# Performance work log

Hardware: AMD Instinct MI355X
Metric: run time of the kernel (lower is better)

The kernel has to match this reference:

```python
import jax, jax.numpy as jnp
import numpy as np

EPS = 1e-5  # BatchNorm eps


def _unfold3x3(x):
    """torch.nn.Unfold(kernel=3, pad=1, stride=1) -> [B, H*W, 9, C] layout.

    Kernel positions are row-major (kh, kw); index 4 is the center, matching
    x_pn[:, :, 4:5, :] in the torch module.
    """
    B, C, H, W = x.shape
    xp = jnp.pad(x, ((0, 0), (0, 0), (1, 1), (1, 1)))
    patches = jnp.stack([xp[:, :, i:i + H, j:j + W]
                         for i in range(3) for j in range(3)], axis=1)  # [B,9,C,H,W]
    return patches.transpose(0, 3, 4, 1, 2).reshape(B, H * W, 9, C)


def setup_inputs() -> dict:
    key = jax.random.key(0)
    ks = jax.random.split(key, 10)
    B, Cin, Cout, H, W = 2, 64, 64, 64, 2048
    Ctot = 4 + Cin  # 4 meta channels + feature channels
    return {
        "x": jax.random.normal(ks[0], (B, Ctot, H, W), jnp.float32),
        "mask": jax.random.randint(ks[1], (B, 1, H, W), 0, 2, jnp.int32),
        # weight_mlp1: Linear(4 -> Cin, bias=False), torch layout [out, in]
        "W1": jax.random.normal(ks[2], (Cin, 4), jnp.float32) * 0.3,
        "bn1_g": jnp.ones((Cin,), jnp.float32),
        "bn1_b": jnp.zeros((Cin,), jnp.float32),
        "bn1_m": jax.random.normal(ks[3], (Cin,), jnp.float32) * 0.1,
        "bn1_v": jax.random.uniform(ks[4], (Cin,), jnp.float32, 0.5, 1.5),
        # weight_mlp2: Linear(Cin -> 1) (attention head)
        "W2": jax.random.normal(ks[5], (1, Cin), jnp.float32) * 0.1,
        "b2": jnp.zeros((1,), jnp.float32),
        # aggregation_mlp: Linear(9*Cin -> Cout, bias=False)
        "Wagg": jax.random.normal(ks[6], (Cout, 9 * Cin), jnp.float32) * 0.04,
        "bn2_g": jnp.ones((Cout,), jnp.float32),
        "bn2_b": jnp.zeros((Cout,), jnp.float32),
        "bn2_m": jax.random.normal(ks[7], (Cout,), jnp.float32) * 0.1,
        "bn2_v": jax.random.uniform(ks[8], (Cout,), jnp.float32, 0.5, 1.5),
    }


def reference(x, mask, W1, bn1_g, bn1_b, bn1_m, bn1_v, W2, b2,
              Wagg, bn2_g, bn2_b, bn2_m, bn2_v):
    B, Ctot, H, W_ = x.shape
    Cin = W1.shape[0]

    xu = _unfold3x3(x)                       # [B, HW, 9, Ctot]
    feats = xu[..., 4:]                      # [B, HW, 9, Cin]
    pn = xu[..., :4]                         # meta coords of 9 neighbors
    d = pn - pn[:, :, 4:5, :]                # relative to center pixel

    # per-neighbor weight MLP (Linear -> BN(eval) -> ReLU -> Linear)
    w = jnp.einsum('bnkm,cm->bnkc', d, W1)   # [B, HW, 9, Cin]
    w = (w - bn1_m) * (bn1_g * jax.lax.rsqrt(bn1_v + EPS)) + bn1_b
    w = jax.nn.relu(w)
    w = jnp.einsum('bnkc,oc->bnko', w, W2) + b2  # [B, HW, 9, 1]

    mu = _unfold3x3(mask.astype(jnp.float32))    # [B, HW, 9, 1]
    w = w * mu                                   # masked logits
    w = jax.nn.softmax(w[..., 0], axis=-1)[..., None]  # attention over 9 neighbors

    out = (w * feats).reshape(B, H * W_, 9 * Cin)
    y = jnp.einsum('bnf,of->bno', out, Wagg)     # [B, HW, Cout]
    y = (y - bn2_m) * (bn2_g * jax.lax.rsqrt(bn2_v + EPS)) + bn2_b
    y = jax.nn.relu(y)
    # Fold(kernel=1) == reshape back to the feature map
    return y.transpose(0, 2, 1).reshape(B, -1, H, W_)
```

## Files before the change

### kernel.cpp

```cpp
#include <hip/hip_runtime.h>

#define H_ 64
#define W_ 2048
#define HWsz (H_*W_)
#define CIN 64
#define CTOT 68
#define COUT 64

typedef float  f32x4  __attribute__((ext_vector_type(4)));
typedef float  f32x16 __attribute__((ext_vector_type(16)));
typedef short  s16x8  __attribute__((ext_vector_type(8)));

__device__ __forceinline__ unsigned short f2bf(float f) {
    unsigned u = __builtin_bit_cast(unsigned, f);
    unsigned r = u + 0x7fffu + ((u >> 16) & 1u);
    return (unsigned short)(r >> 16);
}

__global__ __launch_bounds__(256) void prep_bw(
    const float* __restrict__ Wagg, unsigned short* __restrict__ BwS)
{
    int idx = blockIdx.x * 256 + threadIdx.x;
    if (idx >= 4608) return;
    int lane = idx & 63;
    int rest = idx >> 6;
    int nt = rest & 1;
    int ks = (rest >> 1) & 3;
    int k9 = rest >> 3;
    int o  = nt*32 + (lane & 31);
    int ch = ks*16 + (lane >> 5)*8;
    const float* src = Wagg + (size_t)o*(9*CIN) + k9*64 + ch;
    s16x8 v8;
#pragma unroll
    for (int j = 0; j < 8; ++j) v8[j] = (short)f2bf(src[j]);
    *(s16x8*)(BwS + (size_t)idx*8) = v8;
}

__global__ __launch_bounds__(256, 4) void wsoft_k(
    const float* __restrict__ x, const int* __restrict__ mask,
    const float* __restrict__ W1, const float* __restrict__ g1,
    const float* __restrict__ b1, const float* __restrict__ m1,
    const float* __restrict__ v1, const float* __restrict__ W2,
    const float* __restrict__ b2p, float* __restrict__ wbuf)
{
    __shared__ float pos[3][4][260];
    __shared__ float musk[3][260];
    __shared__ float Wc[64][8];

    int tid = threadIdx.x;
    int bx = blockIdx.x, by = blockIdx.y;
    int b = by >> 6, h = by & 63;
    int w0 = bx << 8;
    const float* xb = x + (size_t)b * CTOT * HWsz;

#pragma unroll
    for (int it = 0; it < 3; ++it) {
        int i = it*256 + tid;
        int grp = i & 63;
        int rc = i >> 6;
        int ch = rc & 3, r = rc >> 2;
        int gr = h - 1 + r;
        float4 v = {0.f, 0.f, 0.f, 0.f};
        if ((unsigned)gr < (unsigned)H_)
            v = *(const float4*)(xb + (size_t)ch*HWsz + (size_t)gr*W_ + w0 + grp*4);
        float* dst = &pos[r][ch][1 + grp*4];
        dst[0] = v.x; dst[1] = v.y; dst[2] = v.z; dst[3] = v.w;
    }
    if (tid < 192) {
        int grp = tid & 63, r = tid >> 6;
        int gr = h - 1 + r;
        float4 mv = {0.f, 0.f, 0.f, 0.f};
        if ((unsigned)gr < (unsigned)H_) {
            const int* mp = mask + ((size_t)b*H_ + gr)*W_ + w0 + grp*4;
            mv.x = (float)mp[0]; mv.y = (float)mp[1]; mv.z = (float)mp[2]; mv.w = (float)mp[3];
        }
        float* dst = &musk[r][1 + grp*4];
        dst[0] = mv.x; dst[1] = mv.y; dst[2] = mv.z; dst[3] = mv.w;
    }
    if (tid < 24) {
        int c2 = tid & 1;
        int rc = tid >> 1; int ch = rc & 3, r = rc >> 2;
        int gr = h - 1 + r, gc = w0 - 1 + c2*257;
        float v = 0.f;
        if (((unsigned)gr < (unsigned)H_) && ((unsigned)gc < (unsigned)W_))
            v = xb[(size_t)ch*HWsz + (size_t)gr*W_ + gc];
        pos[r][ch][c2*257] = v;
    }
    if (tid >= 32 && tid < 38) {
        int t = tid - 32;
        int c2 = t & 1, r = t >> 1;
        int gr = h - 1 + r, gc = w0 - 1 + c2*257;
        float v = 0.f;
        if (((unsigned)gr < (unsigned)H_) && ((unsigned)gc < (unsigned)W_))
            v = (float)mask[((size_t)b*H_ + gr)*W_ + gc];
        musk[r][c2*257] = v;
    }
    if (tid >= 64 && tid < 128) {
        int c = tid - 64;
        float s1 = g1[c] * rsqrtf(v1[c] + 1e-5f);
#pragma unroll
        for (int m = 0; m < 4; ++m) Wc[c][m] = W1[c*4 + m] * s1;
        Wc[c][4] = b1[c] - m1[c]*s1;
        Wc[c][5] = W2[c];
    }
    __syncthreads();

    int px = tid;
    float pc[4];
#pragma unroll
    for (int m = 0; m < 4; ++m) pc[m] = pos[1][m][1 + px];
    float d[9][4], mu[9];
#pragma unroll
    for (int k = 0; k < 9; ++k) {
        int r = k/3, dw = k%3 - 1;
#pragma unroll
        for (int m = 0; m < 4; ++m) d[k][m] = pos[r][m][1 + px + dw] - pc[m];
        mu[k] = musk[r][1 + px + dw];
    }

    float lg[9];
#pragma unroll
    for (int k = 0; k < 9; ++k) lg[k] = 0.f;

#pragma unroll 4
    for (int c = 0; c < CIN; ++c) {
        f32x4 wv = *(const f32x4*)&Wc[c][0];
        float t1c = Wc[c][4], w2c = Wc[c][5];
#pragma unroll
        for (int k = 0; k < 9; ++k) {
            float v = fmaf(d[k][0], wv[0], fmaf(d[k][1], wv[1],
                      fmaf(d[k][2], wv[2], fmaf(d[k][3], wv[3], t1c))));
            lg[k] += fmaxf(v, 0.f) * w2c;
        }
    }

    float b2v = b2p[0];
    float mx = -1e30f;
#pragma unroll
    for (int k = 0; k < 9; ++k) { lg[k] = (lg[k] + b2v) * mu[k]; mx = fmaxf(mx, lg[k]); }
    float s = 0.f, e[9];
#pragma unroll
    for (int k = 0; k < 9; ++k) { e[k] = __expf(lg[k] - mx); s += e[k]; }
    float inv = 1.f / s;
#pragma unroll
    for (int k = 0; k < 9; ++k)
        wbuf[((size_t)by*9 + k)*W_ + w0 + px] = e[k] * inv;
}

__global__ __launch_bounds__(256, 4) void agg_k(
    const float* __restrict__ x,
    const unsigned short* __restrict__ BwS,
    const float* __restrict__ wbuf,
    const float* __restrict__ g2, const float* __restrict__ bb2,
    const float* __restrict__ m2, const float* __restrict__ v2,
    float* __restrict__ out)
{
    __shared__ __align__(16) unsigned short fe[3][8][66][8];

    int tid = threadIdx.x;
    int bx = blockIdx.x, by = blockIdx.y;
    int b = by >> 6, h = by & 63;
    int w0 = bx << 6;
    const float* xf = x + ((size_t)b*CTOT + 4) * HWsz;

#pragma unroll
    for (int it = 0; it < 6; ++it) {
        int i = it*256 + tid;
        int col = i & 63;
        int rg = i >> 6;
        int g = rg & 7, r = rg >> 3;
        int gr = h - 1 + r;
        s16x8 v8 = {0,0,0,0,0,0,0,0};
        if ((unsigned)gr < (unsigned)H_) {
            const float* src = xf + (size_t)(g*8)*HWsz + (size_t)gr*W_ + w0 + col;
#pragma unroll
            for (int j = 0; j < 8; ++j) v8[j] = (short)f2bf(src[(size_t)j*HWsz]);
        }
        *(s16x8*)&fe[r][g][1 + col][0] = v8;
    }
    if (tid < 48) {
        int c2 = tid & 1;
        int rg = tid >> 1;
        int g = rg & 7, r = rg >> 3;
        int gr = h - 1 + r;
        int gc = w0 - 1 + c2*65;
        s16x8 v8 = {0,0,0,0,0,0,0,0};
        if (((unsigned)gr < (unsigned)H_) && ((unsigned)gc < (unsigned)W_)) {
            const float* src = xf + (size_t)(g*8)*HWsz + (size_t)gr*W_ + gc;
#pragma unroll
            for (int j = 0; j < 8; ++j) v8[j] = (short)f2bf(src[(size_t)j*HWsz]);
        }
        *(s16x8*)&fe[r][g][c2*65][0] = v8;
    }
    __syncthreads();

    int lane = tid & 63, wv = tid >> 6;
    int nt = wv & 1, mq = wv >> 1;
    int l31 = lane & 31, l5 = lane >> 5;

    f32x16 fin = {0.f,0.f,0.f,0.f,0.f,0.f,0.f,0.f,0.f,0.f,0.f,0.f,0.f,0.f,0.f,0.f};
    const float* wrow = wbuf + (size_t)by*9*W_ + w0 + mq*32 + 4*l5;

#pragma unroll
    for (int k9 = 0; k9 < 9; ++k9) {
        const int r = k9/3, dw = k9%3 - 1;
        int col = 1 + mq*32 + l31 + dw;

        s16x8 bf[4], af[4];
#pragma unroll
        for (int ks = 0; ks < 4; ++ks)
            bf[ks] = *(const s16x8*)(BwS + (size_t)((((k9<<2) + ks)*2 + nt) << 9) + lane*8);
#pragma unroll
        for (int ks = 0; ks < 4; ++ks)
            af[ks] = *(const s16x8*)&fe[r][ks*2 + l5][col][0];

        f32x16 tmp = {0.f,0.f,0.f,0.f,0.f,0.f,0.f,0.f,0.f,0.f,0.f,0.f,0.f,0.f,0.f,0.f};
#pragma unroll
        for (int ks = 0; ks < 4; ++ks)
            tmp = __builtin_amdgcn_mfma_f32_32x32x16_bf16(af[ks], bf[ks], tmp, 0, 0, 0);

        const float* wk = wrow + (size_t)k9*W_;
        f32x4 a0 = *(const f32x4*)(wk);
        f32x4 a1 = *(const f32x4*)(wk + 8);
        f32x4 a2 = *(const f32x4*)(wk + 16);
        f32x4 a3 = *(const f32x4*)(wk + 24);
#pragma unroll
        for (int c = 0; c < 4; ++c) {
            fin[c]      += a0[c] * tmp[c];
            fin[4 + c]  += a1[c] * tmp[4 + c];
            fin[8 + c]  += a2[c] * tmp[8 + c];
            fin[12 + c] += a3[c] * tmp[12 + c];
        }
    }

    int o = nt*32 + l31;
    float sc = g2[o] * rsqrtf(v2[o] + 1e-5f);
    float tc = bb2[o] - m2[o]*sc;
    float* orow = out + (((size_t)b*COUT + o)*H_ + h)*W_ + w0 + mq*32 + 4*l5;
#pragma unroll
    for (int v = 0; v < 4; ++v) {
        f32x4 q;
#pragma unroll
        for (int c = 0; c < 4; ++c) q[c] = fmaxf(fmaf(fin[4*v + c], sc, tc), 0.f);
        *(f32x4*)(orow + 8*v) = q;
    }
}

extern "C" void kernel_launch(void* const* d_in, const int* in_sizes, int n_in,
                              void* d_out, int out_size, void* d_ws, size_t ws_size,
                              hipStream_t stream)
{
    const float* x    = (const float*)d_in[0];
    const int*   mask = (const int*)d_in[1];
    const float* W1   = (const float*)d_in[2];
    const float* g1   = (const float*)d_in[3];
    const float* b1   = (const float*)d_in[4];
    const float* m1   = (const float*)d_in[5];
    const float* v1   = (const float*)d_in[6];
    const float* W2   = (const float*)d_in[7];
    const float* b2   = (const float*)d_in[8];
    const float* Wagg = (const float*)d_in[9];
    const float* g2   = (const float*)d_in[10];
    const float* bb2  = (const float*)d_in[11];
    const float* m2   = (const float*)d_in[12];
    const float* v2   = (const float*)d_in[13];
    float* outp = (float*)d_out;

    char* ws = (char*)d_ws;
    unsigned short* BwS = (unsigned short*)(ws + 0);
    float* wbuf = (float*)(ws + 131072);

    hipLaunchKernelGGL(prep_bw, dim3(18), dim3(256), 0, stream, Wagg, BwS);
    hipLaunchKernelGGL(wsoft_k, dim3(W_/256, 128), dim3(256), 0, stream,
                       x, mask, W1, g1, b1, m1, v1, W2, b2, wbuf);
    hipLaunchKernelGGL(agg_k, dim3(W_/64, 128), dim3(256), 0, stream,
                       x, BwS, wbuf, g2, bb2, m2, v2, outp);
}
```

Before: 228.8 us.

## Pre-pack features into padded bf16 channel-grouped layout and widen aggregation tiles

Adds a prep kernel that converts the feature channels into a zero-padded bf16 layout grouped by 8 channels. A new aggregation kernel then loads these tiles straight into LDS with global_load_lds, with no per-element conversion or bounds checks, and covers 128 columns per block. It also skips the center-neighbor MLP in wsoft_k, because d=0 there gives a constant logit that is precomputed per channel. The cost is an extra full pass over x (read fp32, write bf16) plus a roughly 35MB workspace, and the old path is kept as a fallback when the workspace is too small.

```diff
diff --git a/kernel.cpp b/kernel.cpp
--- a/kernel.cpp
+++ b/kernel.cpp
@@ -6,6 +6,9 @@
 #define CIN 64
 #define CTOT 68
 #define COUT 64
+
+#define XH 66
+#define XW 2050
 
 typedef float  f32x4  __attribute__((ext_vector_type(4)));
 typedef float  f32x16 __attribute__((ext_vector_type(16)));
@@ -36,6 +39,28 @@
     *(s16x8*)(BwS + (size_t)idx*8) = v8;
 }
 
+__global__ __launch_bounds__(256) void prep_x(
+    const float* __restrict__ x, unsigned short* __restrict__ xpad)
+{
+    int wc = blockIdx.x * 256 + threadIdx.x;
+    if (wc >= XW) return;
+    int hr = blockIdx.y;
+    int b  = blockIdx.z;
+    bool interior = (hr >= 1) && (hr <= H_) && (wc >= 1) && (wc <= W_);
+    const float* src0 = x + ((size_t)b*CTOT + 4)*HWsz + (size_t)(hr-1)*W_ + (wc-1);
+    unsigned short* dst0 = xpad + ((((size_t)b*XH + hr)*8)*XW + wc)*8;
+#pragma unroll
+    for (int g = 0; g < 8; ++g) {
+        s16x8 v8 = {0,0,0,0,0,0,0,0};
+        if (interior) {
+            const float* s = src0 + (size_t)(g*8)*HWsz;
+#pragma unroll
+            for (int j = 0; j < 8; ++j) v8[j] = (short)f2bf(s[(size_t)j*HWsz]);
+        }
+        *(s16x8*)(dst0 + (size_t)g*XW*8) = v8;
+    }
+}
+
 __global__ __launch_bounds__(256, 4) void wsoft_k(
     const float* __restrict__ x, const int* __restrict__ mask,
     const float* __restrict__ W1, const float* __restrict__ g1,
@@ -100,8 +125,12 @@
         float s1 = g1[c] * rsqrtf(v1[c] + 1e-5f);
 #pragma unroll
         for (int m = 0; m < 4; ++m) Wc[c][m] = W1[c*4 + m] * s1;
-        Wc[c][4] = b1[c] - m1[c]*s1;
-        Wc[c][5] = W2[c];
+        float t1c = b1[c] - m1[c]*s1;
+        float w2c = W2[c];
+        Wc[c][4] = t1c;
+        Wc[c][5] = w2c;
+        Wc[c][6] = fmaxf(t1c, 0.f) * w2c;
+        Wc[c][7] = 0.f;
     }
     __syncthreads();
 
@@ -121,18 +150,22 @@
     float lg[9];
 #pragma unroll
     for (int k = 0; k < 9; ++k) lg[k] = 0.f;
+    float lg4 = 0.f;
 
 #pragma unroll 4
     for (int c = 0; c < CIN; ++c) {
         f32x4 wv = *(const f32x4*)&Wc[c][0];
-        float t1c = Wc[c][4], w2c = Wc[c][5];
-#pragma unroll
-        for (int k = 0; k < 9; ++k) {
+        f32x4 w2 = *(const f32x4*)&Wc[c][4];
+        lg4 += w2[2];
+#pragma unroll
+        for (int kk = 0; kk < 8; ++kk) {
+            const int k = kk + (kk >= 4);
             float v = fmaf(d[k][0], wv[0], fmaf(d[k][1], wv[1],
-                      fmaf(d[k][2], wv[2], fmaf(d[k][3], wv[3], t1c))));
-            lg[k] += fmaxf(v, 0.f) * w2c;
-        }
-    }
+                      fmaf(d[k][2], wv[2], fmaf(d[k][3], wv[3], w2[0]))));
+            lg[k] += fmaxf(v, 0.f) * w2[1];
+        }
+    }
+    lg[4] = lg4;
 
     float b2v = b2p[0];
     float mx = -1e30f;
@@ -145,6 +178,99 @@
 #pragma unroll
     for (int k = 0; k < 9; ++k)
         wbuf[((size_t)by*9 + k)*W_ + w0 + px] = e[k] * inv;
+}
+
+__global__ __launch_bounds__(256, 3) void agg_k2(
+    const unsigned short* __restrict__ xpad,
+    const unsigned short* __restrict__ BwS,
+    const float* __restrict__ wbuf,
+    const float* __restrict__ g2, const float* __restrict__ bb2,
+    const float* __restrict__ m2, const float* __restrict__ v2,
+    float* __restrict__ out)
+{
+    __shared__ __align__(16) unsigned short fe[3][8][130][8];
+
+    int tid = threadIdx.x;
+    int bx = blockIdx.x, by = blockIdx.y;
+    int b = by >> 6, h = by & 63;
+    int w0 = bx << 7;
+    int lane = tid & 63, wv = tid >> 6;
+
+    const unsigned short* xb = xpad + (size_t)b*XH*8*XW*8;
+
+#pragma unroll
+    for (int it = 0; it < 12; ++it) {
+        int u = it*4 + wv;
+        int chunk = u & 1, g = (u >> 1) & 7, r = u >> 4;
+        const unsigned short* gsrc =
+            xb + ((((size_t)(h + r)*8 + g)*XW) + w0 + 1 + chunk*64 + lane)*8;
+        unsigned short* ldst = &fe[r][g][1 + chunk*64][0];
+        __builtin_amdgcn_global_load_lds(
+            (const __attribute__((address_space(1))) unsigned int*)gsrc,
+            (__attribute__((address_space(3))) unsigned int*)ldst, 16, 0, 0);
+    }
+    if (tid < 48) {
+        int c2 = tid & 1, g = (tid >> 1) & 7, r = tid >> 4;
+        int wc = w0 + c2*129;
+        s16x8 v8 = *(const s16x8*)(xb + ((((size_t)(h + r)*8 + g)*XW) + wc)*8);
+        *(s16x8*)&fe[r][g][c2*129][0] = v8;
+    }
+    __syncthreads();
+
+    int nt = wv & 1, mh = wv >> 1;
+    int l31 = lane & 31, l5 = lane >> 5;
+
+    const f32x16 fz16 = {0.f,0.f,0.f,0.f,0.f,0.f,0.f,0.f,0.f,0.f,0.f,0.f,0.f,0.f,0.f,0.f};
+    f32x16 fin[2] = {fz16, fz16};
+    const float* wrow = wbuf + (size_t)by*9*W_ + w0 + mh*64 + 4*l5;
+
+#pragma unroll
+    for (int k9 = 0; k9 < 9; ++k9) {
+        const int r = k9/3, dw = k9%3 - 1;
+
+        s16x8 bf[4];
+#pragma unroll
+        for (int ks = 0; ks < 4; ++ks)
+            bf[ks] = *(const s16x8*)(BwS + (size_t)((((k9<<2) + ks)*2 + nt) << 9) + lane*8);
+
+        const float* wk = wrow + (size_t)k9*W_;
+#pragma unroll
+        for (int half = 0; half < 2; ++half) {
+            int j0 = 1 + mh*64 + half*32 + l31 + dw;
+            f32x16 tmp = fz16;
+#pragma unroll
+            for (int ks = 0; ks < 4; ++ks) {
+                s16x8 af = *(const s16x8*)&fe[r][ks*2 + l5][j0][0];
+                tmp = __builtin_amdgcn_mfma_f32_32x32x16_bf16(af, bf[ks], tmp, 0, 0, 0);
+            }
+            f32x4 a0 = *(const f32x4*)(wk + half*32);
+            f32x4 a1 = *(const f32x4*)(wk + half*32 + 8);
+            f32x4 a2 = *(const f32x4*)(wk + half*32 + 16);
+            f32x4 a3 = *(const f32x4*)(wk + half*32 + 24);
+#pragma unroll
+            for (int c = 0; c < 4; ++c) {
+                fin[half][c]      += a0[c] * tmp[c];
+                fin[half][4 + c]  += a1[c] * tmp[4 + c];
+                fin[half][8 + c]  += a2[c] * tmp[8 + c];
+                fin[half][12 + c] += a3[c] * tmp[12 + c];
+            }
+        }
+    }
+
+    int o = nt*32 + l31;
+    float sc = g2[o] * rsqrtf(v2[o] + 1e-5f);
+    float tc = bb2[o] - m2[o]*sc;
+#pragma unroll
+    for (int half = 0; half < 2; ++half) {
+        float* orow = out + (((size_t)b*COUT + o)*H_ + h)*W_ + w0 + mh*64 + half*32 + 4*l5;
+#pragma unroll
+        for (int v = 0; v < 4; ++v) {
+            f32x4 q;
+#pragma unroll
+            for (int c = 0; c < 4; ++c) q[c] = fmaxf(fmaf(fin[half][4*v + c], sc, tc), 0.f);
+            *(f32x4*)(orow + 8*v) = q;
+        }
+    }
 }
 
 __global__ __launch_bounds__(256, 4) void agg_k(
@@ -267,12 +393,29 @@
     float* outp = (float*)d_out;
 
     char* ws = (char*)d_ws;
-    unsigned short* BwS = (unsigned short*)(ws + 0);
-    float* wbuf = (float*)(ws + 131072);
-
-    hipLaunchKernelGGL(prep_bw, dim3(18), dim3(256), 0, stream, Wagg, BwS);
-    hipLaunchKernelGGL(wsoft_k, dim3(W_/256, 128), dim3(256), 0, stream,
-                       x, mask, W1, g1, b1, m1, v1, W2, b2, wbuf);
-    hipLaunchKernelGGL(agg_k, dim3(W_/64, 128), dim3(256), 0, stream,
-                       x, BwS, wbuf, g2, bb2, m2, v2, outp);
-}
+    const size_t xpadBytes = (size_t)2*XH*8*XW*8*2;
+    const size_t bwOff  = 34637824;
+    const size_t wbOff  = bwOff + 131072;
+    const size_t need   = wbOff + (size_t)2*64*9*W_*4;
+    (void)xpadBytes;
+
+    if (ws_size >= need) {
+        unsigned short* xpad = (unsigned short*)(ws + 0);
+        unsigned short* BwS  = (unsigned short*)(ws + bwOff);
+        float*          wbuf = (float*)(ws + wbOff);
+        hipLaunchKernelGGL(prep_bw, dim3(18), dim3(256), 0, stream, Wagg, BwS);
+        hipLaunchKernelGGL(prep_x, dim3((XW + 255)/256, XH, 2), dim3(256), 0, stream, x, xpad);
+        hipLaunchKernelGGL(wsoft_k, dim3(W_/256, 128), dim3(256), 0, stream,
+                           x, mask, W1, g1, b1, m1, v1, W2, b2, wbuf);
+        hipLaunchKernelGGL(agg_k2, dim3(W_/128, 128), dim3(256), 0, stream,
+                           xpad, BwS, wbuf, g2, bb2, m2, v2, outp);
+    } else {
+        unsigned short* BwS  = (unsigned short*)(ws + 0);
+        float*          wbuf = (float*)(ws + 131072);
+        hipLaunchKernelGGL(prep_bw, dim3(18), dim3(256), 0, stream, Wagg, BwS);
+        hipLaunchKernelGGL(wsoft_k, dim3(W_/256, 128), dim3(256), 0, stream,
+                           x, mask, W1, g1, b1, m1, v1, W2, b2, wbuf);
+        hipLaunchKernelGGL(agg_k, dim3(W_/64, 128), dim3(256), 0, stream,
+                           x, BwS, wbuf, g2, bb2, m2, v2, outp);
+    }
+}
```

Result: faster. 217.8 us (-4.8%).

## Fuse attention-softmax and aggregation kernels using padded bf16 channel-packed input

Applied to the files above, without the earlier changes.

Adds a pre-pass that converts features to a zero-padded bf16 channel-grouped layout and pads the position and mask channels. A single fused kernel then computes the per-neighbor logits, skips the center neighbor (its logit is a precomputed constant), runs the softmax in shared memory, and does the MFMA aggregation. Tiles are widened to 128 pixels, and features are loaded into LDS with async global_load_lds. This removes the wbuf round trip and the repeated bf16 conversion of the halo, at the cost of an extra full-tensor transcode pass and lower occupancy.

```diff
diff --git a/kernel.cpp b/kernel.cpp
--- a/kernel.cpp
+++ b/kernel.cpp
@@ -7,6 +7,9 @@
 #define CTOT 68
 #define COUT 64
 
+#define XH 66
+#define XW 2050
+
 typedef float  f32x4  __attribute__((ext_vector_type(4)));
 typedef float  f32x16 __attribute__((ext_vector_type(16)));
 typedef short  s16x8  __attribute__((ext_vector_type(8)));
@@ -18,231 +21,243 @@
 }
 
 __global__ __launch_bounds__(256) void prep_bw(
-    const float* __restrict__ Wagg, unsigned short* __restrict__ BwS)
-{
-    int idx = blockIdx.x * 256 + threadIdx.x;
-    if (idx >= 4608) return;
-    int lane = idx & 63;
-    int rest = idx >> 6;
-    int nt = rest & 1;
-    int ks = (rest >> 1) & 3;
-    int k9 = rest >> 3;
-    int o  = nt*32 + (lane & 31);
-    int ch = ks*16 + (lane >> 5)*8;
-    const float* src = Wagg + (size_t)o*(9*CIN) + k9*64 + ch;
-    s16x8 v8;
-#pragma unroll
-    for (int j = 0; j < 8; ++j) v8[j] = (short)f2bf(src[j]);
-    *(s16x8*)(BwS + (size_t)idx*8) = v8;
-}
-
-__global__ __launch_bounds__(256, 4) void wsoft_k(
-    const float* __restrict__ x, const int* __restrict__ mask,
+    const float* __restrict__ Wagg,
     const float* __restrict__ W1, const float* __restrict__ g1,
     const float* __restrict__ b1, const float* __restrict__ m1,
     const float* __restrict__ v1, const float* __restrict__ W2,
-    const float* __restrict__ b2p, float* __restrict__ wbuf)
-{
-    __shared__ float pos[3][4][260];
-    __shared__ float musk[3][260];
-    __shared__ float Wc[64][8];
+    unsigned short* __restrict__ BwS, float* __restrict__ Wfold)
+{
+    int tid = threadIdx.x;
+    if (blockIdx.x == 0) {
+        if (tid < 64) {
+            float s1 = g1[tid] * rsqrtf(v1[tid] + 1e-5f);
+#pragma unroll
+            for (int m = 0; m < 4; ++m) Wfold[tid*8 + m] = W1[tid*4 + m] * s1;
+            Wfold[tid*8 + 4] = b1[tid] - m1[tid]*s1;
+            Wfold[tid*8 + 5] = W2[tid];
+            Wfold[tid*8 + 6] = 0.f;
+            Wfold[tid*8 + 7] = 0.f;
+        }
+        __syncthreads();
+        if (tid == 0) {
+            float s = 0.f;
+            for (int c = 0; c < 64; ++c) s += fmaxf(Wfold[c*8 + 4], 0.f) * Wfold[c*8 + 5];
+            Wfold[512] = s;
+        }
+    }
+    int idx = blockIdx.x * 256 + tid;
+    if (idx < 4608) {
+        int lane = idx & 63;
+        int rest = idx >> 6;
+        int nt = rest & 1;
+        int ks = (rest >> 1) & 3;
+        int k9 = rest >> 3;
+        int o  = nt*32 + (lane & 31);
+        int ch = ks*16 + (lane >> 5)*8;
+        const float* src = Wagg + (size_t)o*(9*CIN) + k9*64 + ch;
+        s16x8 v8;
+#pragma unroll
+        for (int j = 0; j < 8; ++j) v8[j] = (short)f2bf(src[j]);
+        *(s16x8*)(BwS + (size_t)idx*8) = v8;
+    }
+}
+
+__global__ __launch_bounds__(256) void prep_xpm(
+    const float* __restrict__ x, const int* __restrict__ mask,
+    unsigned short* __restrict__ xpad,
+    float* __restrict__ pospad, float* __restrict__ maskpad)
+{
+    int wc = blockIdx.x * 256 + threadIdx.x;
+    if (wc >= XW) return;
+    int hr = blockIdx.y;
+    int b  = blockIdx.z;
+    bool interior = (hr >= 1) && (hr <= H_) && (wc >= 1) && (wc <= W_);
+    const float* srcf = x + ((size_t)b*CTOT + 4)*HWsz + (size_t)(hr-1)*W_ + (wc-1);
+    unsigned short* dst0 = xpad + ((((size_t)b*XH + hr)*8)*XW + wc)*8;
+#pragma unroll
+    for (int g = 0; g < 8; ++g) {
+        s16x8 v8 = {0,0,0,0,0,0,0,0};
+        if (interior) {
+            const float* s = srcf + (size_t)(g*8)*HWsz;
+#pragma unroll
+            for (int j = 0; j < 8; ++j) v8[j] = (short)f2bf(s[(size_t)j*HWsz]);
+        }
+        *(s16x8*)(dst0 + (size_t)g*XW*8) = v8;
+    }
+    const float* srcp = x + (size_t)b*CTOT*HWsz + (size_t)(hr-1)*W_ + (wc-1);
+#pragma unroll
+    for (int ch = 0; ch < 4; ++ch) {
+        float v = interior ? srcp[(size_t)ch*HWsz] : 0.f;
+        pospad[(((size_t)b*XH + hr)*4 + ch)*XW + wc] = v;
+    }
+    float mv = interior ? (float)mask[((size_t)b*H_ + (hr-1))*W_ + (wc-1)] : 0.f;
+    maskpad[((size_t)b*XH + hr)*XW + wc] = mv;
+}
+
+__global__ __launch_bounds__(256, 2) void fused_k(
+    const unsigned short* __restrict__ xpad,
+    const float* __restrict__ pospad, const float* __restrict__ maskpad,
+    const unsigned short* __restrict__ BwS, const float* __restrict__ Wfold,
+    const float* __restrict__ b2p,
+    const float* __restrict__ g2, const float* __restrict__ bb2,
+    const float* __restrict__ m2, const float* __restrict__ v2,
+    float* __restrict__ out)
+{
+    __shared__ __align__(16) unsigned short fe[3][8][130][8];
+    __shared__ __align__(16) float sw[9][128];
 
     int tid = threadIdx.x;
     int bx = blockIdx.x, by = blockIdx.y;
     int b = by >> 6, h = by & 63;
-    int w0 = bx << 8;
-    const float* xb = x + (size_t)b * CTOT * HWsz;
-
-#pragma unroll
-    for (int it = 0; it < 3; ++it) {
-        int i = it*256 + tid;
-        int grp = i & 63;
-        int rc = i >> 6;
-        int ch = rc & 3, r = rc >> 2;
-        int gr = h - 1 + r;
-        float4 v = {0.f, 0.f, 0.f, 0.f};
-        if ((unsigned)gr < (unsigned)H_)
-            v = *(const float4*)(xb + (size_t)ch*HWsz + (size_t)gr*W_ + w0 + grp*4);
-        float* dst = &pos[r][ch][1 + grp*4];
-        dst[0] = v.x; dst[1] = v.y; dst[2] = v.z; dst[3] = v.w;
-    }
-    if (tid < 192) {
-        int grp = tid & 63, r = tid >> 6;
-        int gr = h - 1 + r;
-        float4 mv = {0.f, 0.f, 0.f, 0.f};
-        if ((unsigned)gr < (unsigned)H_) {
-            const int* mp = mask + ((size_t)b*H_ + gr)*W_ + w0 + grp*4;
-            mv.x = (float)mp[0]; mv.y = (float)mp[1]; mv.z = (float)mp[2]; mv.w = (float)mp[3];
-        }
-        float* dst = &musk[r][1 + grp*4];
-        dst[0] = mv.x; dst[1] = mv.y; dst[2] = mv.z; dst[3] = mv.w;
-    }
-    if (tid < 24) {
-        int c2 = tid & 1;
-        int rc = tid >> 1; int ch = rc & 3, r = rc >> 2;
-        int gr = h - 1 + r, gc = w0 - 1 + c2*257;
-        float v = 0.f;
-        if (((unsigned)gr < (unsigned)H_) && ((unsigned)gc < (unsigned)W_))
-            v = xb[(size_t)ch*HWsz + (size_t)gr*W_ + gc];
-        pos[r][ch][c2*257] = v;
-    }
-    if (tid >= 32 && tid < 38) {
-        int t = tid - 32;
-        int c2 = t & 1, r = t >> 1;
-        int gr = h - 1 + r, gc = w0 - 1 + c2*257;
-        float v = 0.f;
-        if (((unsigned)gr < (unsigned)H_) && ((unsigned)gc < (unsigned)W_))
-            v = (float)mask[((size_t)b*H_ + gr)*W_ + gc];
-        musk[r][c2*257] = v;
-    }
-    if (tid >= 64 && tid < 128) {
-        int c = tid - 64;
-        float s1 = g1[c] * rsqrtf(v1[c] + 1e-5f);
-#pragma unroll
-        for (int m = 0; m < 4; ++m) Wc[c][m] = W1[c*4 + m] * s1;
-        Wc[c][4] = b1[c] - m1[c]*s1;
-        Wc[c][5] = W2[c];
-    }
+    int w0 = bx << 7;
+    int lane = tid & 63, wv = tid >> 6;
+
+    const unsigned short* xb = xpad + (size_t)b*XH*8*XW*8;
+
+#pragma unroll
+    for (int it = 0; it < 12; ++it) {
+        int u = it*4 + wv;
+        int chunk = u & 1, g = (u >> 1) & 7, r = u >> 4;
+        const unsigned short* gsrc =
+            xb + ((((size_t)(h + r)*8 + g)*XW) + w0 + 1 + chunk*64 + lane)*8;
+        unsigned short* ldst = &fe[r][g][1 + chunk*64][0];
+        __builtin_amdgcn_global_load_lds(
+            (const __attribute__((address_space(1))) unsigned int*)gsrc,
+            (__attribute__((address_space(3))) unsigned int*)ldst, 16, 0, 0);
+    }
+    s16x8 haloV = {0,0,0,0,0,0,0,0};
+    int hg = 0, hr3 = 0, hc2 = 0;
+    if (tid < 48) {
+        hc2 = tid & 1; hg = (tid >> 1) & 7; hr3 = tid >> 4;
+        haloV = *(const s16x8*)(xb + ((((size_t)(h + hr3)*8 + hg)*XW) + w0 + hc2*129)*8);
+    }
+
+    int px = tid & 127, kh = tid >> 7;
+    int gw = w0 + px;
+    float pA[4][3], pB[4], pc[4], mu[4];
+    {
+        int rowA = h + (kh ? 2 : 0);
+#pragma unroll
+        for (int ch = 0; ch < 4; ++ch) {
+            const float* pr = pospad + (((size_t)b*XH + rowA)*4 + ch)*XW + gw;
+            pA[ch][0] = pr[0]; pA[ch][1] = pr[1]; pA[ch][2] = pr[2];
+            const float* p1 = pospad + (((size_t)b*XH + h + 1)*4 + ch)*XW + gw;
+            pB[ch] = p1[2*kh];
+            pc[ch] = p1[1];
+        }
+        const float* mr0 = maskpad + ((size_t)b*XH + rowA)*XW + gw;
+        const float* mr1 = maskpad + ((size_t)b*XH + h + 1)*XW + gw;
+        if (kh == 0) {
+            mu[0] = mr0[0]; mu[1] = mr0[1]; mu[2] = mr0[2]; mu[3] = mr1[0];
+        } else {
+            mu[0] = mr1[2]; mu[1] = mr0[0]; mu[2] = mr0[1]; mu[3] = mr0[2];
+        }
+    }
+    float dd[4][4];
+#pragma unroll
+    for (int m = 0; m < 4; ++m) {
+        if (kh == 0) {
+            dd[0][m] = pA[m][0] - pc[m]; dd[1][m] = pA[m][1] - pc[m];
+            dd[2][m] = pA[m][2] - pc[m]; dd[3][m] = pB[m]    - pc[m];
+        } else {
+            dd[0][m] = pB[m]    - pc[m]; dd[1][m] = pA[m][0] - pc[m];
+            dd[2][m] = pA[m][1] - pc[m]; dd[3][m] = pA[m][2] - pc[m];
+        }
+    }
+
+    float lg[4] = {0.f, 0.f, 0.f, 0.f};
+    const f32x4* Wf4 = (const f32x4*)Wfold;
+#pragma unroll 8
+    for (int c = 0; c < CIN; ++c) {
+        f32x4 wa = Wf4[2*c];
+        f32x4 wb = Wf4[2*c + 1];
+#pragma unroll
+        for (int t = 0; t < 4; ++t) {
+            float v = fmaf(dd[t][0], wa[0], fmaf(dd[t][1], wa[1],
+                      fmaf(dd[t][2], wa[2], fmaf(dd[t][3], wa[3], wb[0]))));
+            lg[t] += fmaxf(v, 0.f) * wb[1];
+        }
+    }
+    float b2v = b2p[0];
+#pragma unroll
+    for (int t = 0; t < 4; ++t) {
+        int k = kh ? (5 + t) : t;
+        sw[k][px] = (lg[t] + b2v) * mu[t];
+    }
+    if (tid < 48) *(s16x8*)&fe[hr3][hg][hc2*129][0] = haloV;
     __syncthreads();
 
-    int px = tid;
-    float pc[4];
-#pragma unroll
-    for (int m = 0; m < 4; ++m) pc[m] = pos[1][m][1 + px];
-    float d[9][4], mu[9];
-#pragma unroll
-    for (int k = 0; k < 9; ++k) {
-        int r = k/3, dw = k%3 - 1;
-#pragma unroll
-        for (int m = 0; m < 4; ++m) d[k][m] = pos[r][m][1 + px + dw] - pc[m];
-        mu[k] = musk[r][1 + px + dw];
-    }
-
-    float lg[9];
-#pragma unroll
-    for (int k = 0; k < 9; ++k) lg[k] = 0.f;
-
-#pragma unroll 4
-    for (int c = 0; c < CIN; ++c) {
-        f32x4 wv = *(const f32x4*)&Wc[c][0];
-        float t1c = Wc[c][4], w2c = Wc[c][5];
-#pragma unroll
-        for (int k = 0; k < 9; ++k) {
-            float v = fmaf(d[k][0], wv[0], fmaf(d[k][1], wv[1],
-                      fmaf(d[k][2], wv[2], fmaf(d[k][3], wv[3], t1c))));
-            lg[k] += fmaxf(v, 0.f) * w2c;
-        }
-    }
-
-    float b2v = b2p[0];
-    float mx = -1e30f;
-#pragma unroll
-    for (int k = 0; k < 9; ++k) { lg[k] = (lg[k] + b2v) * mu[k]; mx = fmaxf(mx, lg[k]); }
-    float s = 0.f, e[9];
-#pragma unroll
-    for (int k = 0; k < 9; ++k) { e[k] = __expf(lg[k] - mx); s += e[k]; }
-    float inv = 1.f / s;
-#pragma unroll
-    for (int k = 0; k < 9; ++k)
-        wbuf[((size_t)by*9 + k)*W_ + w0 + px] = e[k] * inv;
-}
-
-__global__ __launch_bounds__(256, 4) void agg_k(
-    const float* __restrict__ x,
-    const unsigned short* __restrict__ BwS,
-    const float* __restrict__ wbuf,
-    const float* __restrict__ g2, const float* __restrict__ bb2,
-    const float* __restrict__ m2, const float* __restrict__ v2,
-    float* __restrict__ out)
-{
-    __shared__ __align__(16) unsigned short fe[3][8][66][8];
-
-    int tid = threadIdx.x;
-    int bx = blockIdx.x, by = blockIdx.y;
-    int b = by >> 6, h = by & 63;
-    int w0 = bx << 6;
-    const float* xf = x + ((size_t)b*CTOT + 4) * HWsz;
-
-#pragma unroll
-    for (int it = 0; it < 6; ++it) {
-        int i = it*256 + tid;
-        int col = i & 63;
-        int rg = i >> 6;
-        int g = rg & 7, r = rg >> 3;
-        int gr = h - 1 + r;
-        s16x8 v8 = {0,0,0,0,0,0,0,0};
-        if ((unsigned)gr < (unsigned)H_) {
-            const float* src = xf + (size_t)(g*8)*HWsz + (size_t)gr*W_ + w0 + col;
-#pragma unroll
-            for (int j = 0; j < 8; ++j) v8[j] = (short)f2bf(src[(size_t)j*HWsz]);
-        }
-        *(s16x8*)&fe[r][g][1 + col][0] = v8;
-    }
-    if (tid < 48) {
-        int c2 = tid & 1;
-        int rg = tid >> 1;
-        int g = rg & 7, r = rg >> 3;
-        int gr = h - 1 + r;
-        int gc = w0 - 1 + c2*65;
-        s16x8 v8 = {0,0,0,0,0,0,0,0};
-        if (((unsigned)gr < (unsigned)H_) && ((unsigned)gc < (unsigned)W_)) {
-            const float* src = xf + (size_t)(g*8)*HWsz + (size_t)gr*W_ + gc;
-#pragma unroll
-            for (int j = 0; j < 8; ++j) v8[j] = (short)f2bf(src[(size_t)j*HWsz]);
-        }
-        *(s16x8*)&fe[r][g][c2*65][0] = v8;
+    if (tid < 128) {
+        int p2 = tid, g2w = w0 + p2;
+        float mu4 = maskpad[((size_t)b*XH + h + 1)*XW + g2w + 1];
+        float lgv[9];
+#pragma unroll
+        for (int k = 0; k < 9; ++k) if (k != 4) lgv[k] = sw[k][p2];
+        lgv[4] = (Wfold[512] + b2v) * mu4;
+        float mx = -1e30f;
+#pragma unroll
+        for (int k = 0; k < 9; ++k) mx = fmaxf(mx, lgv[k]);
+        float s = 0.f, e[9];
+#pragma unroll
+        for (int k = 0; k < 9; ++k) { e[k] = __expf(lgv[k] - mx); s += e[k]; }
+        float inv = 1.f / s;
+#pragma unroll
+        for (int k = 0; k < 9; ++k) sw[k][p2] = e[k] * inv;
     }
     __syncthreads();
 
-    int lane = tid & 63, wv = tid >> 6;
-    int nt = wv & 1, mq = wv >> 1;
+    int nt = wv & 1, mh = wv >> 1;
     int l31 = lane & 31, l5 = lane >> 5;
 
-    f32x16 fin = {0.f,0.f,0.f,0.f,0.f,0.f,0.f,0.f,0.f,0.f,0.f,0.f,0.f,0.f,0.f,0.f};
-    const float* wrow = wbuf + (size_t)by*9*W_ + w0 + mq*32 + 4*l5;
+    const f32x16 fz16 = {0.f,0.f,0.f,0.f,0.f,0.f,0.f,0.f,0.f,0.f,0.f,0.f,0.f,0.f,0.f,0.f};
+    f32x16 fin[2] = {fz16, fz16};
 
 #pragma unroll
     for (int k9 = 0; k9 < 9; ++k9) {
         const int r = k9/3, dw = k9%3 - 1;
-        int col = 1 + mq*32 + l31 + dw;
-
-        s16x8 bf[4], af[4];
+
+        s16x8 bf[4];
 #pragma unroll
         for (int ks = 0; ks < 4; ++ks)
             bf[ks] = *(const s16x8*)(BwS + (size_t)((((k9<<2) + ks)*2 + nt) << 9) + lane*8);
-#pragma unroll
-        for (int ks = 0; ks < 4; ++ks)
-            af[ks] = *(const s16x8*)&fe[r][ks*2 + l5][col][0];
-
-        f32x16 tmp = {0.f,0.f,0.f,0.f,0.f,0.f,0.f,0.f,0.f,0.f,0.f,0.f,0.f,0.f,0.f,0.f};
-#pragma unroll
-        for (int ks = 0; ks < 4; ++ks)
-            tmp = __builtin_amdgcn_mfma_f32_32x32x16_bf16(af[ks], bf[ks], tmp, 0, 0, 0);
-
-        const float* wk = wrow + (size_t)k9*W_;
-        f32x4 a0 = *(const f32x4*)(wk);
-        f32x4 a1 = *(const f32x4*)(wk + 8);
-        f32x4 a2 = *(const f32x4*)(wk + 16);
-        f32x4 a3 = *(const f32x4*)(wk + 24);
-#pragma unroll
-        for (int c = 0; c < 4; ++c) {
-            fin[c]      += a0[c] * tmp[c];
-            fin[4 + c]  += a1[c] * tmp[4 + c];
-            fin[8 + c]  += a2[c] * tmp[8 + c];
-            fin[12 + c] += a3[c] * tmp[12 + c];
+
+#pragma unroll
+        for (int half = 0; half < 2; ++half) {
+            int j0 = 1 + mh*64 + half*32 + l31 + dw;
+            f32x16 tmp = fz16;
+#pragma unroll
+            for (int ks = 0; ks < 4; ++ks) {
+                s16x8 af = *(const s16x8*)&fe[r][ks*2 + l5][j0][0];
+                tmp = __builtin_amdgcn_mfma_f32_32x32x16_bf16(af, bf[ks], tmp, 0, 0, 0);
+            }
+            int wbase = mh*64 + half*32 + 4*l5;
+            f32x4 a0 = *(const f32x4*)&sw[k9][wbase];
+            f32x4 a1 = *(const f32x4*)&sw[k9][wbase + 8];
+            f32x4 a2 = *(const f32x4*)&sw[k9][wbase + 16];
+            f32x4 a3 = *(const f32x4*)&sw[k9][wbase + 24];
+#pragma unroll
+            for (int c = 0; c < 4; ++c) {
+                fin[half][c]      += a0[c] * tmp[c];
+                fin[half][4 + c]  += a1[c] * tmp[4 + c];
+                fin[half][8 + c]  += a2[c] * tmp[8 + c];
+                fin[half][12 + c] += a3[c] * tmp[12 + c];
+            }
         }
     }
 
     int o = nt*32 + l31;
     float sc = g2[o] * rsqrtf(v2[o] + 1e-5f);
     float tc = bb2[o] - m2[o]*sc;
-    float* orow = out + (((size_t)b*COUT + o)*H_ + h)*W_ + w0 + mq*32 + 4*l5;
-#pragma unroll
-    for (int v = 0; v < 4; ++v) {
-        f32x4 q;
-#pragma unroll
-        for (int c = 0; c < 4; ++c) q[c] = fmaxf(fmaf(fin[4*v + c], sc, tc), 0.f);
-        *(f32x4*)(orow + 8*v) = q;
+#pragma unroll
+    for (int half = 0; half < 2; ++half) {
+        float* orow = out + (((size_t)b*COUT + o)*H_ + h)*W_ + w0 + mh*64 + half*32 + 4*l5;
+#pragma unroll
+        for (int v = 0; v < 4; ++v) {
+            f32x4 q;
+#pragma unroll
+            for (int c = 0; c < 4; ++c) q[c] = fmaxf(fmaf(fin[half][4*v + c], sc, tc), 0.f);
+            *(f32x4*)(orow + 8*v) = q;
+        }
     }
 }
 
@@ -267,12 +282,17 @@
     float* outp = (float*)d_out;
 
     char* ws = (char*)d_ws;
-    unsigned short* BwS = (unsigned short*)(ws + 0);
-    float* wbuf = (float*)(ws + 131072);
-
-    hipLaunchKernelGGL(prep_bw, dim3(18), dim3(256), 0, stream, Wagg, BwS);
-    hipLaunchKernelGGL(wsoft_k, dim3(W_/256, 128), dim3(256), 0, stream,
-                       x, mask, W1, g1, b1, m1, v1, W2, b2, wbuf);
-    hipLaunchKernelGGL(agg_k, dim3(W_/64, 128), dim3(256), 0, stream,
-                       x, BwS, wbuf, g2, bb2, m2, v2, outp);
-}
+    unsigned short* xpad    = (unsigned short*)(ws + 0);
+    float*          pospad  = (float*)(ws + 34636800);
+    float*          maskpad = (float*)(ws + 38966400);
+    unsigned short* BwS     = (unsigned short*)(ws + 40048800);
+    float*          Wfold   = (float*)(ws + 40122528);
+
+    hipLaunchKernelGGL(prep_bw, dim3(18), dim3(256), 0, stream,
+                       Wagg, W1, g1, b1, m1, v1, W2, BwS, Wfold);
+    hipLaunchKernelGGL(prep_xpm, dim3((XW + 255)/256, XH, 2), dim3(256), 0, stream,
+                       x, mask, xpad, pospad, maskpad);
+    hipLaunchKernelGGL(fused_k, dim3(W_/128, 128), dim3(256), 0, stream,
+                       xpad, pospad, maskpad, BwS, Wfold, b2,
+                       g2, bb2, m2, v2, outp);
+}
```

Result: faster. 207.3 us (-9.4%).
